# Kernel optimization log

Measured on AMD Instinct MI355X. Metric: run time of the kernel, lower is better.

## Reference

```python
import jax, jax.numpy as jnp
import numpy as np

B, S, D, H = 4, 2048, 1024, 16
HD = D // H
SCALE = HD ** -0.5


def setup_inputs() -> dict:
    key = jax.random.key(0)
    ks = jax.random.split(key, 5)
    std = D ** -0.5
    return {
        "x": jax.random.normal(ks[0], (B, S, D), jnp.float32),
        "wq": jax.random.normal(ks[1], (D, D), jnp.float32) * std,
        "bq": jnp.zeros((D,), jnp.float32),
        "wk": jax.random.normal(ks[2], (D, D), jnp.float32) * std,
        "bk": jnp.zeros((D,), jnp.float32),
        "wv": jax.random.normal(ks[3], (D, D), jnp.float32) * std,
        "bv": jnp.zeros((D,), jnp.float32),
        "wo": jax.random.normal(ks[4], (D, D), jnp.float32) * std,
        "bo": jnp.zeros((D,), jnp.float32),
    }


def reference(x, wq, bq, wk, bk, wv, bv, wo, bo):
    # projections; weights stored as [in, out] so y = x @ w + b
    q = (x @ wq + bq).reshape(B, S, H, HD).transpose(0, 2, 1, 3)  # [B,H,S,HD]
    k = (x @ wk + bk).reshape(B, S, H, HD).transpose(0, 2, 1, 3)
    v = (x @ wv + bv).reshape(B, S, H, HD).transpose(0, 2, 1, 3)
    attn = jnp.einsum("bhqd,bhkd->bhqk", q, k) * SCALE  # [B,H,S,S]
    attn = jax.nn.softmax(attn, axis=-1)
    out = jnp.einsum("bhqk,bhkd->bhqd", attn, v)  # [B,H,S,HD]
    out = out.transpose(0, 2, 1, 3).reshape(B, S, D)
    return out @ wo + bo
```

## Files before the change

kernel.cpp:

```cpp
#include <hip/hip_runtime.h>
#include <stdint.h>


typedef __attribute__((ext_vector_type(8))) short bf16x8;
typedef __attribute__((ext_vector_type(4))) short bf16x4;
typedef __attribute__((ext_vector_type(4))) float f32x4;
typedef __attribute__((ext_vector_type(16))) float f32x16;
typedef __attribute__((ext_vector_type(4))) int i32x4;
typedef unsigned short u16;
typedef unsigned int u32;

#define AS1 __attribute__((address_space(1)))
#define AS3 __attribute__((address_space(3)))

#define SCALE_L2E 0.18033688011112042f

__device__ __forceinline__ void gld_lds16(const void* g, void* l) {
  __builtin_amdgcn_global_load_lds((const AS1 void*)g, (AS3 void*)l, 16, 0, 0);
}

__device__ __forceinline__ u16 f2bf(float f) {
  u32 x = __builtin_bit_cast(u32, f);
  x += 0x7fff + ((x >> 16) & 1);
  return (u16)(x >> 16);
}

__device__ __forceinline__ u16 f2bf_fast(float a) {
#if __has_builtin(__builtin_amdgcn_cvt_pk_bf16_f32)
  auto v = __builtin_amdgcn_cvt_pk_bf16_f32(a, a);
  return (u16)(__builtin_bit_cast(u32, v) & 0xffffu);
#else
  return f2bf(a);
#endif
}

__device__ __forceinline__ u32 pk2(float a, float b) {
#if __has_builtin(__builtin_amdgcn_cvt_pk_bf16_f32)
  return __builtin_bit_cast(u32, __builtin_amdgcn_cvt_pk_bf16_f32(a, b));
#else
  return (u32)f2bf(a) | ((u32)f2bf(b) << 16);
#endif
}

__device__ __forceinline__ float exp2_fast(float x) {
#if __has_builtin(__builtin_amdgcn_exp2f)
  return __builtin_amdgcn_exp2f(x);
#else
  return exp2f(x);
#endif
}

__device__ __forceinline__ f32x16 zero16() {
  f32x16 z;
#pragma unroll
  for (int i = 0; i < 16; ++i) z[i] = 0.f;
  return z;
}

__global__ __launch_bounds__(256) void convert_x(const float* __restrict__ x,
                                                 u16* __restrict__ xb) {
  int i = (blockIdx.x * 256 + threadIdx.x) * 4;
  float4 v = *(const float4*)(x + i);
  ushort4 o;
  o.x = f2bf(v.x); o.y = f2bf(v.y); o.z = f2bf(v.z); o.w = f2bf(v.w);
  *(ushort4*)(xb + i) = o;
}

__global__ __launch_bounds__(256) void pack_weights(
    const float* __restrict__ wq, const float* __restrict__ wk,
    const float* __restrict__ wv, const float* __restrict__ wo,
    u16* __restrict__ wt_qkv, u16* __restrict__ wt_o) {
  __shared__ float tile[64][65];
  int mat = blockIdx.z;
  const float* src = (mat == 0) ? wq : (mat == 1) ? wk : (mat == 2) ? wv : wo;
  int k0 = blockIdx.y * 64, j0 = blockIdx.x * 64;
  int t = threadIdx.x;
  int lr = t >> 6;
  int lc = t & 63;
#pragma unroll
  for (int it = 0; it < 16; ++it) {
    int r = it * 4 + lr;
    tile[r][lc] = src[(size_t)(k0 + r) * 1024 + j0 + lc];
  }
  __syncthreads();
  u16* dst = (mat == 3) ? wt_o : (wt_qkv + (size_t)mat * 1024 * 1024);
#pragma unroll
  for (int it = 0; it < 16; ++it) {
    int nl = it * 4 + lr;
    float v = tile[lc][nl];
    if (mat == 0) v *= SCALE_L2E;
    dst[(size_t)(j0 + nl) * 1024 + k0 + lc] = f2bf(v);
  }
}

template <int MODE>
__global__ __launch_bounds__(256, 2) void gemm_bt(
    const u16* __restrict__ A, const u16* __restrict__ Bt,
    const float* __restrict__ bias0, const float* __restrict__ bias1,
    const float* __restrict__ bias2,
    void* __restrict__ out0v, void* __restrict__ out1v, void* __restrict__ out2v) {
  __shared__ u16 lA[128 * 32];
  __shared__ u16 lB[128 * 32];
  const int K = 1024;
  int tid = threadIdx.x;
  int wave = tid >> 6, lane = tid & 63;

  int bid = blockIdx.x;
  int m0, n0;
  if constexpr (MODE == 0) {
    int xcd = bid & 7, j = bid >> 3;
    n0 = (xcd * 3 + j % 3) * 128;
    m0 = (j / 3) * 128;
  } else {
    n0 = (bid & 7) * 128;
    m0 = (bid >> 3) * 128;
  }
  int wm = (wave & 1) * 64, wn = (wave >> 1) * 64;

  f32x4 acc[4][4];
#pragma unroll
  for (int i = 0; i < 4; ++i)
#pragma unroll
    for (int j = 0; j < 4; ++j) acc[i][j] = f32x4{0.f, 0.f, 0.f, 0.f};

  int srow = lane >> 2;
  int scol = (lane & 3) * 8;

  for (int k0 = 0; k0 < K; k0 += 32) {
#pragma unroll
    for (int c = 0; c < 2; ++c) {
      int rbase = wave * 32 + c * 16;
      gld_lds16(A + (size_t)(m0 + rbase + srow) * K + k0 + scol, lA + rbase * 32);
      gld_lds16(Bt + (size_t)(n0 + rbase + srow) * K + k0 + scol, lB + rbase * 32);
    }
    __syncthreads();
    bf16x8 af[4], bfr[4];
#pragma unroll
    for (int mt = 0; mt < 4; ++mt)
      af[mt] = *(const bf16x8*)(lA + (wm + mt * 16 + (lane & 15)) * 32 + (lane >> 4) * 8);
#pragma unroll
    for (int nt = 0; nt < 4; ++nt)
      bfr[nt] = *(const bf16x8*)(lB + (wn + nt * 16 + (lane & 15)) * 32 + (lane >> 4) * 8);
#pragma unroll
    for (int mt = 0; mt < 4; ++mt)
#pragma unroll
      for (int nt = 0; nt < 4; ++nt)
        acc[mt][nt] = __builtin_amdgcn_mfma_f32_16x16x32_bf16(af[mt], bfr[nt], acc[mt][nt], 0, 0, 0);
    __syncthreads();
  }

  int rbase0 = m0 + wm + (lane >> 4) * 4;
  int cbase = n0 + wn + (lane & 15);
#pragma unroll
  for (int nt = 0; nt < 4; ++nt) {
    int col = cbase + nt * 16;
    if constexpr (MODE == 0) {
      int mat = col >> 10, j = col & 1023;
      const float* bp = (mat == 0) ? bias0 : (mat == 1) ? bias1 : bias2;
      float bv = bp[j];
      if (mat == 0) bv *= SCALE_L2E;
      if (mat == 2) {
        int h = j >> 6, hd = j & 63;
        u16* base = (u16*)out2v;
#pragma unroll
        for (int mt = 0; mt < 4; ++mt) {
          int row0 = rbase0 + mt * 16;
          int b = row0 >> 11, s = row0 & 2047;
          int ci = s >> 6, sg = (s >> 2) & 15;
          int slot = (hd + 4 * sg) & 63;
          size_t off = (size_t)(b * 16 + h) * 131072 + ci * 4096 + sg * 256 + slot * 4;
          ushort4 pk;
          pk.x = f2bf_fast(acc[mt][nt][0] + bv);
          pk.y = f2bf_fast(acc[mt][nt][1] + bv);
          pk.z = f2bf_fast(acc[mt][nt][2] + bv);
          pk.w = f2bf_fast(acc[mt][nt][3] + bv);
          *(ushort4*)(base + off) = pk;
        }
      } else {
        u16* base = (mat == 0) ? (u16*)out0v : (u16*)out1v;
#pragma unroll
        for (int mt = 0; mt < 4; ++mt)
#pragma unroll
          for (int r = 0; r < 4; ++r) {
            int row = rbase0 + mt * 16 + r;
            base[(size_t)row * 1024 + j] = f2bf_fast(acc[mt][nt][r] + bv);
          }
      }
    } else {
      float bv = bias0[col];
      float* o = (float*)out0v;
#pragma unroll
      for (int mt = 0; mt < 4; ++mt)
#pragma unroll
        for (int r = 0; r < 4; ++r) {
          int row = rbase0 + mt * 16 + r;
          o[(size_t)row * 1024 + col] = acc[mt][nt][r] + bv;
        }
    }
  }
}

__global__ __launch_bounds__(512, 4) void flash_attn(
    const u16* __restrict__ Q, const u16* __restrict__ Kb,
    const u16* __restrict__ Vg, u16* __restrict__ ctx) {
  __shared__ u16 lK[2][64 * 32];
  __shared__ u16 lV[4096];
  int tid = threadIdx.x, wave = tid >> 6, lane = tid & 63;

  int F = blockIdx.x;
  int xcd = F & 7, idx = F >> 3;
  int bh = xcd * 8 + (idx >> 3);
  int q0 = (idx & 7) * 256;
  int b = bh >> 4, h = bh & 15;
  const u16* Qp = Q + (size_t)b * 2048 * 1024 + h * 64;
  const u16* Kp = Kb + (size_t)b * 2048 * 1024 + h * 64;
  const u16* Vp = Vg + (size_t)bh * 131072;

  int ql = lane & 31;
  int hi = lane >> 5;

  bf16x8 qf[4];
  {
    const u16* qrow = Qp + (size_t)(q0 + wave * 32 + ql) * 1024;
#pragma unroll
    for (int kk = 0; kk < 4; ++kk)
      qf[kk] = *(const bf16x8*)(qrow + kk * 16 + hi * 8);
  }

  float lsum = 0.f;
  f32x16 o[2];
  o[0] = zero16();
  o[1] = zero16();

  int srow = lane >> 2;
  int schunk = (((lane & 3) ^ ((lane >> 3) & 3)) * 8);
  int kk_w = wave & 1;
  int rb = wave >> 1;
  int stg_row = rb * 16 + srow;
  int rkey = ((lane & 15) >> 1) & 3;

  const u16* gK = Kp + (size_t)stg_row * 1024 + kk_w * 32 + schunk;
  const u16* gV = Vp + wave * 512 + lane * 8;
  u16* wK = lK[kk_w] + rb * 512 + lane * 8;
  u16* wV = lV + wave * 512 + lane * 8;

  i32x4 ldK = *(const i32x4*)gK;
  i32x4 ldV = *(const i32x4*)gV;
  *(i32x4*)wK = ldK;
  *(i32x4*)wV = ldV;
  __syncthreads();

  for (int s0 = 0; s0 < 2048; s0 += 64) {
    bool more = (s0 + 64 < 2048);
    if (more) {
      ldK = *(const i32x4*)(gK + (size_t)(s0 + 64) * 1024);
      ldV = *(const i32x4*)(gV + (size_t)(s0 + 64) * 64);
    }

#pragma unroll
    for (int sb = 0; sb < 2; ++sb) {
      bf16x8 kf[4];
      int krb = (sb * 32 + ql) * 32;
#pragma unroll
      for (int kk = 0; kk < 4; ++kk)
        kf[kk] = *(const bf16x8*)(lK[kk >> 1] + krb + ((((kk & 1) << 1) | hi) ^ rkey) * 8);

      f32x16 sa = zero16();
#pragma unroll
      for (int kk = 0; kk < 4; ++kk)
        sa = __builtin_amdgcn_mfma_f32_32x32x16_bf16(kf[kk], qf[kk], sa, 0, 0, 0);

      float p[16];
#pragma unroll
      for (int r = 0; r < 16; ++r) p[r] = exp2_fast(sa[r]);
      {
        float a0 = (p[0] + p[1]) + (p[2] + p[3]);
        float a1 = (p[4] + p[5]) + (p[6] + p[7]);
        float a2 = (p[8] + p[9]) + (p[10] + p[11]);
        float a3 = (p[12] + p[13]) + (p[14] + p[15]);
        lsum += (a0 + a1) + (a2 + a3);
      }

#pragma unroll
      for (int ss = 0; ss < 2; ++ss) {
        union { u32 w[4]; bf16x8 v; } pu;
        pu.w[0] = pk2(p[8 * ss + 0], p[8 * ss + 1]);
        pu.w[1] = pk2(p[8 * ss + 2], p[8 * ss + 3]);
        pu.w[2] = pk2(p[8 * ss + 4], p[8 * ss + 5]);
        pu.w[3] = pk2(p[8 * ss + 6], p[8 * ss + 7]);
        int sgA = sb * 8 + ss * 4 + hi;
        int sgB = sgA + 2;
#pragma unroll
        for (int dh = 0; dh < 2; ++dh) {
          int d = dh * 32 + ql;
          union { bf16x4 half_[2]; bf16x8 v; } vu;
          vu.half_[0] = *(const bf16x4*)(lV + sgA * 256 + (((d + 4 * sgA) & 63) << 2));
          vu.half_[1] = *(const bf16x4*)(lV + sgB * 256 + (((d + 4 * sgB) & 63) << 2));
          o[dh] = __builtin_amdgcn_mfma_f32_32x32x16_bf16(vu.v, pu.v, o[dh], 0, 0, 0);
        }
      }
    }

    __syncthreads();
    if (more) {
      *(i32x4*)wK = ldK;
      *(i32x4*)wV = ldV;
    }
    __syncthreads();
  }

  float rs = lsum + __shfl_xor(lsum, 32);
  float inv = 1.0f / fmaxf(rs, 1e-30f);
  int q = q0 + wave * 32 + ql;
  size_t rowbase = ((size_t)(b * 2048 + q) * 16 + h) * 64;
#pragma unroll
  for (int dh = 0; dh < 2; ++dh)
#pragma unroll
    for (int rr = 0; rr < 4; ++rr) {
      ushort4 pk;
      pk.x = f2bf_fast(o[dh][4 * rr + 0] * inv);
      pk.y = f2bf_fast(o[dh][4 * rr + 1] * inv);
      pk.z = f2bf_fast(o[dh][4 * rr + 2] * inv);
      pk.w = f2bf_fast(o[dh][4 * rr + 3] * inv);
      *(ushort4*)(ctx + rowbase + dh * 32 + rr * 8 + hi * 4) = pk;
    }
}

extern "C" void kernel_launch(void* const* d_in, const int* in_sizes, int n_in,
                              void* d_out, int out_size, void* d_ws, size_t ws_size,
                              hipStream_t stream) {
  const float* x  = (const float*)d_in[0];
  const float* wq = (const float*)d_in[1];
  const float* bq = (const float*)d_in[2];
  const float* wk = (const float*)d_in[3];
  const float* bk = (const float*)d_in[4];
  const float* wv = (const float*)d_in[5];
  const float* bv = (const float*)d_in[6];
  const float* wo = (const float*)d_in[7];
  const float* bo = (const float*)d_in[8];

  u16* ws = (u16*)d_ws;
  u16* xb     = ws;
  u16* wt_qkv = xb + (size_t)8192 * 1024;
  u16* wt_o   = wt_qkv + (size_t)3072 * 1024;
  u16* Qb     = wt_o + (size_t)1024 * 1024;
  u16* Kbuf   = Qb + (size_t)8192 * 1024;
  u16* Vgb    = Kbuf + (size_t)8192 * 1024;
  u16* ctx    = Vgb + (size_t)8192 * 1024;

  convert_x<<<8192, 256, 0, stream>>>(x, xb);
  pack_weights<<<dim3(16, 16, 4), 256, 0, stream>>>(wq, wk, wv, wo, wt_qkv, wt_o);
  gemm_bt<0><<<1536, 256, 0, stream>>>(xb, wt_qkv, bq, bk, bv, Qb, Kbuf, Vgb);
  flash_attn<<<512, 512, 0, stream>>>(Qb, Kbuf, Vgb, ctx);
  gemm_bt<1><<<512, 256, 0, stream>>>(ctx, wt_o, bo, nullptr, nullptr,
                                      d_out, nullptr, nullptr);
}
```

Before: 288.8 us.

## Process two 32-row query tiles per wave in flash attention to reuse K/V

Each wave now handles 64 query rows (two 32-row MFMA tiles) instead of 32, so every K and V fragment read from LDS feeds two MFMAs. The grid is halved to 256 blocks of 512 queries, and launch bounds drop to 2 blocks per CU to allow more registers. The aim is to cut LDS traffic and global K/V reloads per query. The cost is higher register pressure, lower occupancy, and only 256 blocks, which may underfill the 256 CUs' latency hiding.

```diff
diff --git a/kernel.cpp b/kernel.cpp
--- a/kernel.cpp
+++ b/kernel.cpp
@@ -200,7 +200,7 @@
   }
 }
 
-__global__ __launch_bounds__(512, 4) void flash_attn(
+__global__ __launch_bounds__(512, 2) void flash_attn(
     const u16* __restrict__ Q, const u16* __restrict__ Kb,
     const u16* __restrict__ Vg, u16* __restrict__ ctx) {
   __shared__ u16 lK[2][64 * 32];
@@ -209,8 +209,8 @@
 
   int F = blockIdx.x;
   int xcd = F & 7, idx = F >> 3;
-  int bh = xcd * 8 + (idx >> 3);
-  int q0 = (idx & 7) * 256;
+  int bh = xcd * 8 + (idx >> 2);
+  int q0 = (idx & 3) * 512;
   int b = bh >> 4, h = bh & 15;
   const u16* Qp = Q + (size_t)b * 2048 * 1024 + h * 64;
   const u16* Kp = Kb + (size_t)b * 2048 * 1024 + h * 64;
@@ -219,18 +219,21 @@
   int ql = lane & 31;
   int hi = lane >> 5;
 
-  bf16x8 qf[4];
-  {
-    const u16* qrow = Qp + (size_t)(q0 + wave * 32 + ql) * 1024;
+  bf16x8 qf[2][4];
+#pragma unroll
+  for (int qt = 0; qt < 2; ++qt) {
+    const u16* qrow = Qp + (size_t)(q0 + wave * 64 + qt * 32 + ql) * 1024;
 #pragma unroll
     for (int kk = 0; kk < 4; ++kk)
-      qf[kk] = *(const bf16x8*)(qrow + kk * 16 + hi * 8);
-  }
-
-  float lsum = 0.f;
-  f32x16 o[2];
-  o[0] = zero16();
-  o[1] = zero16();
+      qf[qt][kk] = *(const bf16x8*)(qrow + kk * 16 + hi * 8);
+  }
+
+  float lsum[2] = {0.f, 0.f};
+  f32x16 o[2][2];
+#pragma unroll
+  for (int qt = 0; qt < 2; ++qt)
+#pragma unroll
+    for (int dh = 0; dh < 2; ++dh) o[qt][dh] = zero16();
 
   int srow = lane >> 2;
   int schunk = (((lane & 3) ^ ((lane >> 3) & 3)) * 8);
@@ -265,29 +268,38 @@
       for (int kk = 0; kk < 4; ++kk)
         kf[kk] = *(const bf16x8*)(lK[kk >> 1] + krb + ((((kk & 1) << 1) | hi) ^ rkey) * 8);
 
-      f32x16 sa = zero16();
-#pragma unroll
-      for (int kk = 0; kk < 4; ++kk)
-        sa = __builtin_amdgcn_mfma_f32_32x32x16_bf16(kf[kk], qf[kk], sa, 0, 0, 0);
-
-      float p[16];
-#pragma unroll
-      for (int r = 0; r < 16; ++r) p[r] = exp2_fast(sa[r]);
-      {
+      f32x16 sa0 = zero16(), sa1 = zero16();
+#pragma unroll
+      for (int kk = 0; kk < 4; ++kk) {
+        sa0 = __builtin_amdgcn_mfma_f32_32x32x16_bf16(kf[kk], qf[0][kk], sa0, 0, 0, 0);
+        sa1 = __builtin_amdgcn_mfma_f32_32x32x16_bf16(kf[kk], qf[1][kk], sa1, 0, 0, 0);
+      }
+
+      bf16x8 pu[2][2];
+#pragma unroll
+      for (int qt = 0; qt < 2; ++qt) {
+        float p[16];
+#pragma unroll
+        for (int r = 0; r < 16; ++r)
+          p[r] = exp2_fast(qt == 0 ? sa0[r] : sa1[r]);
         float a0 = (p[0] + p[1]) + (p[2] + p[3]);
         float a1 = (p[4] + p[5]) + (p[6] + p[7]);
         float a2 = (p[8] + p[9]) + (p[10] + p[11]);
         float a3 = (p[12] + p[13]) + (p[14] + p[15]);
-        lsum += (a0 + a1) + (a2 + a3);
+        lsum[qt] += (a0 + a1) + (a2 + a3);
+#pragma unroll
+        for (int ss = 0; ss < 2; ++ss) {
+          union { u32 w[4]; bf16x8 v; } pk_;
+          pk_.w[0] = pk2(p[8 * ss + 0], p[8 * ss + 1]);
+          pk_.w[1] = pk2(p[8 * ss + 2], p[8 * ss + 3]);
+          pk_.w[2] = pk2(p[8 * ss + 4], p[8 * ss + 5]);
+          pk_.w[3] = pk2(p[8 * ss + 6], p[8 * ss + 7]);
+          pu[qt][ss] = pk_.v;
+        }
       }
 
 #pragma unroll
       for (int ss = 0; ss < 2; ++ss) {
-        union { u32 w[4]; bf16x8 v; } pu;
-        pu.w[0] = pk2(p[8 * ss + 0], p[8 * ss + 1]);
-        pu.w[1] = pk2(p[8 * ss + 2], p[8 * ss + 3]);
-        pu.w[2] = pk2(p[8 * ss + 4], p[8 * ss + 5]);
-        pu.w[3] = pk2(p[8 * ss + 6], p[8 * ss + 7]);
         int sgA = sb * 8 + ss * 4 + hi;
         int sgB = sgA + 2;
 #pragma unroll
@@ -296,7 +308,8 @@
           union { bf16x4 half_[2]; bf16x8 v; } vu;
           vu.half_[0] = *(const bf16x4*)(lV + sgA * 256 + (((d + 4 * sgA) & 63) << 2));
           vu.half_[1] = *(const bf16x4*)(lV + sgB * 256 + (((d + 4 * sgB) & 63) << 2));
-          o[dh] = __builtin_amdgcn_mfma_f32_32x32x16_bf16(vu.v, pu.v, o[dh], 0, 0, 0);
+          o[0][dh] = __builtin_amdgcn_mfma_f32_32x32x16_bf16(vu.v, pu[0][ss], o[0][dh], 0, 0, 0);
+          o[1][dh] = __builtin_amdgcn_mfma_f32_32x32x16_bf16(vu.v, pu[1][ss], o[1][dh], 0, 0, 0);
         }
       }
     }
@@ -309,21 +322,24 @@
     __syncthreads();
   }
 
-  float rs = lsum + __shfl_xor(lsum, 32);
-  float inv = 1.0f / fmaxf(rs, 1e-30f);
-  int q = q0 + wave * 32 + ql;
-  size_t rowbase = ((size_t)(b * 2048 + q) * 16 + h) * 64;
-#pragma unroll
-  for (int dh = 0; dh < 2; ++dh)
-#pragma unroll
-    for (int rr = 0; rr < 4; ++rr) {
-      ushort4 pk;
-      pk.x = f2bf_fast(o[dh][4 * rr + 0] * inv);
-      pk.y = f2bf_fast(o[dh][4 * rr + 1] * inv);
-      pk.z = f2bf_fast(o[dh][4 * rr + 2] * inv);
-      pk.w = f2bf_fast(o[dh][4 * rr + 3] * inv);
-      *(ushort4*)(ctx + rowbase + dh * 32 + rr * 8 + hi * 4) = pk;
-    }
+#pragma unroll
+  for (int qt = 0; qt < 2; ++qt) {
+    float rs = lsum[qt] + __shfl_xor(lsum[qt], 32);
+    float inv = 1.0f / fmaxf(rs, 1e-30f);
+    int q = q0 + wave * 64 + qt * 32 + ql;
+    size_t rowbase = ((size_t)(b * 2048 + q) * 16 + h) * 64;
+#pragma unroll
+    for (int dh = 0; dh < 2; ++dh)
+#pragma unroll
+      for (int rr = 0; rr < 4; ++rr) {
+        ushort4 pk;
+        pk.x = f2bf_fast(o[qt][dh][4 * rr + 0] * inv);
+        pk.y = f2bf_fast(o[qt][dh][4 * rr + 1] * inv);
+        pk.z = f2bf_fast(o[qt][dh][4 * rr + 2] * inv);
+        pk.w = f2bf_fast(o[qt][dh][4 * rr + 3] * inv);
+        *(ushort4*)(ctx + rowbase + dh * 32 + rr * 8 + hi * 4) = pk;
+      }
+  }
 }
 
 extern "C" void kernel_launch(void* const* d_in, const int* in_sizes, int n_in,
@@ -351,7 +367,7 @@
   convert_x<<<8192, 256, 0, stream>>>(x, xb);
   pack_weights<<<dim3(16, 16, 4), 256, 0, stream>>>(wq, wk, wv, wo, wt_qkv, wt_o);
   gemm_bt<0><<<1536, 256, 0, stream>>>(xb, wt_qkv, bq, bk, bv, Qb, Kbuf, Vgb);
-  flash_attn<<<512, 512, 0, stream>>>(Qb, Kbuf, Vgb, ctx);
+  flash_attn<<<256, 512, 0, stream>>>(Qb, Kbuf, Vgb, ctx);
   gemm_bt<1><<<512, 256, 0, stream>>>(ctx, wt_o, bo, nullptr, nullptr,
                                       d_out, nullptr, nullptr);
 }
```

After: 283.8 us. Within noise of the previous version (-1.7%).
